# Optimization experiments

Measured on AMD Instinct MI355X. Metric: run time of the kernel, lower is better.

## Reference

```python
import jax, jax.numpy as jnp
import numpy as np

HIDDEN = 32
FEATURES = 16
LABELS = 4
T = 8
N = 40000
E = 640000
D_IN = FEATURES + LABELS + HIDDEN + 1  # GATv2Conv input dim = 53


def setup_inputs() -> dict:
    key = jax.random.key(0)
    ks = jax.random.split(key, 16)
    x = jax.random.normal(ks[0], (T, N, FEATURES), dtype=jnp.float32)
    mask = (jax.random.uniform(ks[1], (N,)) < 0.7).astype(jnp.float32)
    labels = jax.random.normal(ks[2], (N, LABELS), dtype=jnp.float32)
    edge_index = jax.random.randint(ks[3], (2, E), 0, N, dtype=jnp.int32)
    edge_weight = jax.random.uniform(ks[4], (E,), dtype=jnp.float32)
    s = 1.0 / np.sqrt(D_IN)
    # 4 GATv2Conv layers stacked: 0=reset, 1=update, 2=cell, 3=final
    Wl = jax.random.normal(ks[5], (4, HIDDEN, D_IN), dtype=jnp.float32) * s
    bl = jnp.zeros((4, HIDDEN), dtype=jnp.float32)
    Wr = jax.random.normal(ks[6], (4, HIDDEN, D_IN), dtype=jnp.float32) * s
    br = jnp.zeros((4, HIDDEN), dtype=jnp.float32)
    att = jax.random.normal(ks[7], (4, HIDDEN), dtype=jnp.float32) * (1.0 / np.sqrt(HIDDEN))
    bconv = jnp.zeros((4, HIDDEN), dtype=jnp.float32)
    W1 = jax.random.normal(ks[8], (FEATURES, HIDDEN), dtype=jnp.float32) * (1.0 / np.sqrt(HIDDEN))
    b1 = jnp.zeros((FEATURES,), dtype=jnp.float32)
    W2 = jax.random.normal(ks[9], (FEATURES, 2 * HIDDEN), dtype=jnp.float32) * (1.0 / np.sqrt(2 * HIDDEN))
    b2 = jnp.zeros((FEATURES,), dtype=jnp.float32)
    return {"x": x, "mask": mask, "labels": labels, "edge_index": edge_index,
            "edge_weight": edge_weight, "Wl": Wl, "bl": bl, "Wr": Wr, "br": br,
            "att": att, "bconv": bconv, "W1": W1, "b1": b1, "W2": W2, "b2": b2}


def gatv2(xin, src, dst, Wl, bl, Wr, br, att, bconv):
    # GATv2Conv, heads=1, add_self_loops=False (edge_weight unused: lin_edge is None)
    xl = xin @ Wl.T + bl          # [N, H] source transform (message)
    xr = xin @ Wr.T + br          # [N, H] target transform
    z = jax.nn.leaky_relu(xl[src] + xr[dst], 0.2)  # [E, H]
    e = z @ att                   # [E] attention logits
    m = jax.ops.segment_max(e, dst, num_segments=N)
    a = jnp.exp(e - m[dst])
    den = jax.ops.segment_sum(a, dst, num_segments=N)[dst]
    a = a / jnp.where(den > 0, den, 1.0)
    out = jax.ops.segment_sum(a[:, None] * xl[src], dst, num_segments=N)
    return out + bconv


def reference(x, mask, labels, edge_index, edge_weight, Wl, bl, Wr, br, att, bconv, W1, b1, W2, b2):
    src, dst = edge_index[0], edge_index[1]
    mcol = mask[:, None]                       # [N, 1] float, concatenated as a feature
    mbool = mcol > 0.5                         # [N, 1] bool, used for where()
    masked_input = jnp.where(mbool[None], x, 0.0)  # [T, N, F]
    hidden0 = jnp.ones((N, HIDDEN), dtype=x.dtype)
    x2_0 = masked_input[0]

    def step(carry, xt):
        hidden, x2 = carry
        ft = jnp.concatenate([x2, mcol, labels], axis=1)        # [N, F+1+L]
        inp = jnp.concatenate([ft, hidden], axis=1)             # [N, D_IN]
        reset = jax.nn.sigmoid(gatv2(inp, src, dst, Wl[0], bl[0], Wr[0], br[0], att[0], bconv[0]))
        update = jax.nn.sigmoid(gatv2(inp, src, dst, Wl[1], bl[1], Wr[1], br[1], att[1], bconv[1]))
        cin = jnp.concatenate([ft, reset * hidden], axis=1)
        cell = jnp.tanh(gatv2(cin, src, dst, Wl[2], bl[2], Wr[2], br[2], att[2], bconv[2]))
        hidden = update * hidden + (1.0 - update) * cell        # (dropout inactive: eval mode)
        y1 = hidden @ W1.T + b1
        x1 = jnp.where(mbool, xt, y1)
        ft2 = jnp.concatenate([x1, mcol, hidden, labels], axis=1)  # [N, D_IN]
        s = jax.nn.relu(gatv2(ft2, src, dst, Wl[3], bl[3], Wr[3], br[3], att[3], bconv[3]))
        y2 = jnp.concatenate([s, hidden], axis=1) @ W2.T + b2
        x2_new = jnp.where(mbool, xt, y2)
        return (hidden, x2_new), x2_new

    _, out = jax.lax.scan(step, (hidden0, x2_0), masked_input)
    return out  # [T, N, F]
```

## Files before the change

kernel.cpp:

```cpp
#include <hip/hip_runtime.h>
#include <math.h>

#define NN   40000
#define EE   640000
#define HID  32
#define FEAT 16
#define LAB  4
#define TT   8
#define DIN  53
#define WD   (HID * DIN)


__global__ __launch_bounds__(256) void zero_i32(int* __restrict__ p, int n) {
    int i = blockIdx.x * 256 + threadIdx.x;
    if (i < n) p[i] = 0;
}

__global__ __launch_bounds__(256) void hist_kernel(const int* __restrict__ dst,
                                                   int* __restrict__ deg) {
    int e = blockIdx.x * 256 + threadIdx.x;
    if (e < EE) atomicAdd(&deg[dst[e]], 1);
}

__global__ __launch_bounds__(1024) void scan_kernel(const int* __restrict__ deg,
                                                    int* __restrict__ row_ptr) {
    __shared__ int wsum[16];
    __shared__ int chunk_total;
    int tid = threadIdx.x;
    int lane = tid & 63, wv = tid >> 6;
    int carry = 0;
    if (tid == 0) row_ptr[0] = 0;
    for (int base = 0; base < NN; base += 1024) {
        int i = base + tid;
        int v = (i < NN) ? deg[i] : 0;
        #pragma unroll
        for (int o = 1; o < 64; o <<= 1) {
            int t = __shfl_up(v, o);
            if (lane >= o) v += t;
        }
        if (lane == 63) wsum[wv] = v;
        __syncthreads();
        if (tid < 16) {
            int s = wsum[tid];
            #pragma unroll
            for (int o = 1; o < 16; o <<= 1) {
                int t = __shfl_up(s, o);
                if (tid >= o) s += t;
            }
            wsum[tid] = s;
            if (tid == 15) chunk_total = s;
        }
        __syncthreads();
        int woff = (wv == 0) ? 0 : wsum[wv - 1];
        if (i < NN) row_ptr[i + 1] = carry + woff + v;
        carry += chunk_total;
        __syncthreads();
    }
}

__global__ __launch_bounds__(256) void scatter_kernel(const int* __restrict__ src,
                                                      const int* __restrict__ dst,
                                                      const int* __restrict__ row_ptr,
                                                      int* __restrict__ cursor,
                                                      int* __restrict__ csr_src) {
    int e = blockIdx.x * 256 + threadIdx.x;
    if (e < EE) {
        int d = dst[e];
        int pos = atomicAdd(&cursor[d], 1);
        csr_src[row_ptr[d] + pos] = src[e];
    }
}


__global__ __launch_bounds__(256) void init_kernel(const float* __restrict__ x0,
                                                   const float* __restrict__ mask,
                                                   float* __restrict__ hidden,
                                                   float* __restrict__ x2) {
    int i = blockIdx.x * 256 + threadIdx.x;
    if (i < NN * HID) hidden[i] = 1.0f;
    if (i < NN * FEAT) {
        int node = i >> 4;
        x2[i] = (mask[node] > 0.5f) ? x0[i] : 0.0f;
    }
}


__global__ __launch_bounds__(256) void dense01_kernel(const float* __restrict__ feat,
                                                      const float* __restrict__ mask,
                                                      const float* __restrict__ labels,
                                                      const float* __restrict__ hsrc,
                                                      const float* __restrict__ Wl,
                                                      const float* __restrict__ bl,
                                                      const float* __restrict__ Wr,
                                                      const float* __restrict__ br,
                                                      float* __restrict__ xl01,
                                                      float* __restrict__ xr01) {
    __shared__ float W_s[4 * WD];
    __shared__ float inp_s[8][DIN];
    for (int idx = threadIdx.x; idx < WD; idx += 256) {
        W_s[idx]          = Wl[idx];
        W_s[WD + idx]     = Wl[WD + idx];
        W_s[2 * WD + idx] = Wr[idx];
        W_s[3 * WD + idx] = Wr[WD + idx];
    }
    int ni = threadIdx.x >> 5, k = threadIdx.x & 31;
    int node = blockIdx.x * 8 + ni;
    for (int i = k; i < DIN; i += 32) {
        float v;
        if (i < 16)       v = feat[node * 16 + i];
        else if (i == 16) v = mask[node];
        else if (i < 21)  v = labels[node * 4 + (i - 17)];
        else              v = hsrc[node * 32 + (i - 21)];
        inp_s[ni][i] = v;
    }
    __syncthreads();
    float l0 = bl[k], l1 = bl[HID + k], r0 = br[k], r1 = br[HID + k];
    const float* w0 = &W_s[k * DIN];
    const float* w1 = &W_s[WD + k * DIN];
    const float* w2 = &W_s[2 * WD + k * DIN];
    const float* w3 = &W_s[3 * WD + k * DIN];
#pragma unroll
    for (int i = 0; i < DIN; ++i) {
        float xv = inp_s[ni][i];
        l0 += xv * w0[i];
        l1 += xv * w1[i];
        r0 += xv * w2[i];
        r1 += xv * w3[i];
    }
    xl01[node * 64 + k]      = l0;
    xl01[node * 64 + 32 + k] = l1;
    xr01[node * 64 + k]      = r0;
    xr01[node * 64 + 32 + k] = r1;
}


__global__ __launch_bounds__(256) void dense_kernel(const float* __restrict__ feat,
                                                    const float* __restrict__ mask,
                                                    const float* __restrict__ labels,
                                                    const float* __restrict__ hsrc,
                                                    const float* __restrict__ hmul,
                                                    const float* __restrict__ Wl,
                                                    const float* __restrict__ bl,
                                                    const float* __restrict__ Wr,
                                                    const float* __restrict__ br,
                                                    float* __restrict__ xl,
                                                    float* __restrict__ xr) {
    __shared__ float Wl_s[WD];
    __shared__ float Wr_s[WD];
    __shared__ float inp_s[8][DIN];
    for (int idx = threadIdx.x; idx < WD; idx += 256) {
        Wl_s[idx] = Wl[idx];
        Wr_s[idx] = Wr[idx];
    }
    int ni = threadIdx.x >> 5, k = threadIdx.x & 31;
    int node = blockIdx.x * 8 + ni;
    for (int i = k; i < DIN; i += 32) {
        float v;
        if (i < 16)       v = feat[node * 16 + i];
        else if (i == 16) v = mask[node];
        else if (i < 21)  v = labels[node * 4 + (i - 17)];
        else              v = hsrc[node * 32 + (i - 21)] * hmul[node * 32 + (i - 21)];
        inp_s[ni][i] = v;
    }
    __syncthreads();
    float al = bl[k], ar = br[k];
    const float* wlr = &Wl_s[k * DIN];
    const float* wrr = &Wr_s[k * DIN];
#pragma unroll
    for (int i = 0; i < DIN; ++i) {
        float xv = inp_s[ni][i];
        al += xv * wlr[i];
        ar += xv * wrr[i];
    }
    xl[node * 32 + k] = al;
    xr[node * 32 + k] = ar;
}


__device__ __forceinline__ float edge_score(const float4& v0, const float4& v1,
                                            const float4& xr0, const float4& xr1,
                                            const float4& at0, const float4& at1) {
    float part, z;
    z = v0.x + xr0.x; z = (z > 0.f) ? z : 0.2f * z; part  = z * at0.x;
    z = v0.y + xr0.y; z = (z > 0.f) ? z : 0.2f * z; part += z * at0.y;
    z = v0.z + xr0.z; z = (z > 0.f) ? z : 0.2f * z; part += z * at0.z;
    z = v0.w + xr0.w; z = (z > 0.f) ? z : 0.2f * z; part += z * at0.w;
    z = v1.x + xr1.x; z = (z > 0.f) ? z : 0.2f * z; part += z * at1.x;
    z = v1.y + xr1.y; z = (z > 0.f) ? z : 0.2f * z; part += z * at1.y;
    z = v1.z + xr1.z; z = (z > 0.f) ? z : 0.2f * z; part += z * at1.z;
    z = v1.w + xr1.w; z = (z > 0.f) ? z : 0.2f * z; part += z * at1.w;
    part += __shfl_xor(part, 1);
    part += __shfl_xor(part, 2);
    return part;
}

__device__ __forceinline__ void online_update(float e, float& m, float& den, float* acc,
                                              const float4& v0, const float4& v1) {
    if (e > m) {
        float sc = __expf(m - e);
        den *= sc;
#pragma unroll
        for (int i = 0; i < 8; ++i) acc[i] *= sc;
        m = e;
    }
    float a = __expf(e - m);
    den += a;
    acc[0] += a * v0.x; acc[1] += a * v0.y; acc[2] += a * v0.z; acc[3] += a * v0.w;
    acc[4] += a * v1.x; acc[5] += a * v1.y; acc[6] += a * v1.z; acc[7] += a * v1.w;
}

__device__ __forceinline__ void merge_groups(float m, float den, const float* acc,
                                             bool nonempty, float* o) {
    if (nonempty) {
        float mt = m;
        mt = fmaxf(mt, __shfl_xor(mt, 4));
        mt = fmaxf(mt, __shfl_xor(mt, 8));
        mt = fmaxf(mt, __shfl_xor(mt, 16));
        mt = fmaxf(mt, __shfl_xor(mt, 32));
        float sc = __expf(m - mt);
        float d = den * sc;
        d += __shfl_xor(d, 4);
        d += __shfl_xor(d, 8);
        d += __shfl_xor(d, 16);
        d += __shfl_xor(d, 32);
#pragma unroll
        for (int i = 0; i < 8; ++i) {
            float t = acc[i] * sc;
            t += __shfl_xor(t, 4);
            t += __shfl_xor(t, 8);
            t += __shfl_xor(t, 16);
            t += __shfl_xor(t, 32);
            o[i] = t / d;
        }
    } else {
#pragma unroll
        for (int i = 0; i < 8; ++i) o[i] = 0.0f;
    }
}


__global__ __launch_bounds__(256) void conv01_kernel(const int* __restrict__ row_ptr,
                                                     const int* __restrict__ csr_src,
                                                     const float* __restrict__ xl01,
                                                     const float* __restrict__ xr01,
                                                     const float* __restrict__ att,
                                                     const float* __restrict__ bconv,
                                                     float* __restrict__ g0,
                                                     float* __restrict__ g1) {
    int wid  = threadIdx.x >> 6;
    int lane = threadIdx.x & 63;
    int g = lane >> 2, j = lane & 3;
    int n = blockIdx.x * 4 + wid;
    int c0 = j * 8;
    int beg = row_ptr[n], end = row_ptr[n + 1];

    float4 a00 = *(const float4*)(att + c0);
    float4 a01 = *(const float4*)(att + c0 + 4);
    float4 a10 = *(const float4*)(att + 32 + c0);
    float4 a11 = *(const float4*)(att + 32 + c0 + 4);
    const float* xrn = xr01 + n * 64;
    float4 xr00 = *(const float4*)(xrn + c0);
    float4 xr01v = *(const float4*)(xrn + c0 + 4);
    float4 xr10 = *(const float4*)(xrn + 32 + c0);
    float4 xr11 = *(const float4*)(xrn + 32 + c0 + 4);

    float m0 = -INFINITY, den0 = 0.0f, acc0[8] = {0, 0, 0, 0, 0, 0, 0, 0};
    float m1 = -INFINITY, den1 = 0.0f, acc1[8] = {0, 0, 0, 0, 0, 0, 0, 0};

    for (int p = beg + g; p < end; p += 16) {
        int s = csr_src[p];
        const float4* rp = (const float4*)(xl01 + s * 64 + c0);
        const float4* rq = (const float4*)(xl01 + s * 64 + 32 + c0);
        float4 v00 = rp[0], v01 = rp[1];
        float4 v10 = rq[0], v11 = rq[1];
        float e0 = edge_score(v00, v01, xr00, xr01v, a00, a01);
        float e1 = edge_score(v10, v11, xr10, xr11, a10, a11);
        online_update(e0, m0, den0, acc0, v00, v01);
        online_update(e1, m1, den1, acc1, v10, v11);
    }

    float o0[8], o1[8];
    bool ne = beg < end;
    merge_groups(m0, den0, acc0, ne, o0);
    merge_groups(m1, den1, acc1, ne, o1);

    if (g == 0) {
        float4 b00 = *(const float4*)(bconv + c0);
        float4 b01 = *(const float4*)(bconv + c0 + 4);
        float4 b10 = *(const float4*)(bconv + 32 + c0);
        float4 b11 = *(const float4*)(bconv + 32 + c0 + 4);
        float r0[8] = {o0[0] + b00.x, o0[1] + b00.y, o0[2] + b00.z, o0[3] + b00.w,
                       o0[4] + b01.x, o0[5] + b01.y, o0[6] + b01.z, o0[7] + b01.w};
        float r1[8] = {o1[0] + b10.x, o1[1] + b10.y, o1[2] + b10.z, o1[3] + b10.w,
                       o1[4] + b11.x, o1[5] + b11.y, o1[6] + b11.z, o1[7] + b11.w};
#pragma unroll
        for (int i = 0; i < 8; ++i) {
            r0[i] = 1.0f / (1.0f + __expf(-r0[i]));
            r1[i] = 1.0f / (1.0f + __expf(-r1[i]));
        }
        float4* p0 = (float4*)(g0 + n * 32 + c0);
        p0[0] = make_float4(r0[0], r0[1], r0[2], r0[3]);
        p0[1] = make_float4(r0[4], r0[5], r0[6], r0[7]);
        float4* p1 = (float4*)(g1 + n * 32 + c0);
        p1[0] = make_float4(r1[0], r1[1], r1[2], r1[3]);
        p1[1] = make_float4(r1[4], r1[5], r1[6], r1[7]);
    }
}


__global__ __launch_bounds__(256) void conv2_kernel(const int* __restrict__ row_ptr,
                                                    const int* __restrict__ csr_src,
                                                    const float* __restrict__ xl,
                                                    const float* __restrict__ xr,
                                                    const float* __restrict__ att,
                                                    const float* __restrict__ bconv,
                                                    float* __restrict__ out) {
    int wid  = threadIdx.x >> 6;
    int lane = threadIdx.x & 63;
    int g = lane >> 2, j = lane & 3;
    int n = blockIdx.x * 4 + wid;
    int c0 = j * 8;
    int beg = row_ptr[n], end = row_ptr[n + 1];

    float4 at0 = *(const float4*)(att + c0);
    float4 at1 = *(const float4*)(att + c0 + 4);
    float4 xr0 = *(const float4*)(xr + n * 32 + c0);
    float4 xr1 = *(const float4*)(xr + n * 32 + c0 + 4);

    float m = -INFINITY, den = 0.0f, acc[8] = {0, 0, 0, 0, 0, 0, 0, 0};
    for (int p = beg + g; p < end; p += 16) {
        int s = csr_src[p];
        const float4* rp = (const float4*)(xl + s * 32 + c0);
        float4 v0 = rp[0], v1 = rp[1];
        float e = edge_score(v0, v1, xr0, xr1, at0, at1);
        online_update(e, m, den, acc, v0, v1);
    }
    float o[8];
    merge_groups(m, den, acc, beg < end, o);

    if (g == 0) {
        float4 bc0 = *(const float4*)(bconv + c0);
        float4 bc1 = *(const float4*)(bconv + c0 + 4);
        float r[8] = {o[0] + bc0.x, o[1] + bc0.y, o[2] + bc0.z, o[3] + bc0.w,
                      o[4] + bc1.x, o[5] + bc1.y, o[6] + bc1.z, o[7] + bc1.w};
#pragma unroll
        for (int i = 0; i < 8; ++i) r[i] = tanhf(r[i]);
        float4* op = (float4*)(out + n * 32 + c0);
        op[0] = make_float4(r[0], r[1], r[2], r[3]);
        op[1] = make_float4(r[4], r[5], r[6], r[7]);
    }
}


__global__ __launch_bounds__(256) void conv3_out_kernel(const int* __restrict__ row_ptr,
                                                        const int* __restrict__ csr_src,
                                                        const float* __restrict__ xl,
                                                        const float* __restrict__ xr,
                                                        const float* __restrict__ att,
                                                        const float* __restrict__ bconv,
                                                        const float* __restrict__ hidden,
                                                        const float* __restrict__ W2,
                                                        const float* __restrict__ b2,
                                                        const float* __restrict__ x_t,
                                                        const float* __restrict__ mask,
                                                        float* __restrict__ x2,
                                                        float* __restrict__ out_t) {
    __shared__ float W2s[64 * 16];
    for (int idx = threadIdx.x; idx < 64 * 16; idx += 256) {
        int f = idx & 15, c = idx >> 4;
        W2s[c * 16 + f] = W2[f * 64 + c];
    }
    __syncthreads();

    int wid  = threadIdx.x >> 6;
    int lane = threadIdx.x & 63;
    int g = lane >> 2, j = lane & 3;
    int n = blockIdx.x * 4 + wid;
    int c0 = j * 8;
    int beg = row_ptr[n], end = row_ptr[n + 1];

    float4 at0 = *(const float4*)(att + c0);
    float4 at1 = *(const float4*)(att + c0 + 4);
    float4 xr0 = *(const float4*)(xr + n * 32 + c0);
    float4 xr1 = *(const float4*)(xr + n * 32 + c0 + 4);

    float m = -INFINITY, den = 0.0f, acc[8] = {0, 0, 0, 0, 0, 0, 0, 0};
    for (int p = beg + g; p < end; p += 16) {
        int s = csr_src[p];
        const float4* rp = (const float4*)(xl + s * 32 + c0);
        float4 v0 = rp[0], v1 = rp[1];
        float e = edge_score(v0, v1, xr0, xr1, at0, at1);
        online_update(e, m, den, acc, v0, v1);
    }
    float o[8];
    merge_groups(m, den, acc, beg < end, o);

    float4 bc0 = *(const float4*)(bconv + c0);
    float4 bc1 = *(const float4*)(bconv + c0 + 4);
    float r[8] = {fmaxf(o[0] + bc0.x, 0.f), fmaxf(o[1] + bc0.y, 0.f),
                  fmaxf(o[2] + bc0.z, 0.f), fmaxf(o[3] + bc0.w, 0.f),
                  fmaxf(o[4] + bc1.x, 0.f), fmaxf(o[5] + bc1.y, 0.f),
                  fmaxf(o[6] + bc1.z, 0.f), fmaxf(o[7] + bc1.w, 0.f)};
    float4 h0 = *(const float4*)(hidden + n * 32 + c0);
    float4 h1 = *(const float4*)(hidden + n * 32 + c0 + 4);
    float hv[8] = {h0.x, h0.y, h0.z, h0.w, h1.x, h1.y, h1.z, h1.w};

    int f = lane & 15;
    int base = lane & ~3;
    float y = b2[f];
#pragma unroll
    for (int j2 = 0; j2 < 4; ++j2) {
#pragma unroll
        for (int i = 0; i < 8; ++i) {
            float sv = __shfl(r[i], base + j2);
            float hh = __shfl(hv[i], base + j2);
            int c = j2 * 8 + i;
            y += sv * W2s[c * 16 + f] + hh * W2s[(32 + c) * 16 + f];
        }
    }
    if (lane < 16) {
        float mv = mask[n];
        float xv = x_t[n * 16 + f];
        float rr = (mv > 0.5f) ? xv : y;
        x2[n * 16 + f] = rr;
        out_t[n * 16 + f] = rr;
    }
}


__global__ __launch_bounds__(256) void update_dense3_kernel(
        const float* __restrict__ g_update, const float* __restrict__ g_cell,
        float* __restrict__ hidden,
        const float* __restrict__ x_t, const float* __restrict__ mask,
        const float* __restrict__ labels,
        const float* __restrict__ W1, const float* __restrict__ b1,
        const float* __restrict__ Wl3, const float* __restrict__ bl3,
        const float* __restrict__ Wr3, const float* __restrict__ br3,
        float* __restrict__ xl, float* __restrict__ xr) {
    __shared__ float Wl_s[WD];
    __shared__ float Wr_s[WD];
    __shared__ float W1_s[FEAT * HID];
    __shared__ float inp_s[8][DIN];
    __shared__ float hs[8][HID + 1];
    for (int idx = threadIdx.x; idx < WD; idx += 256) {
        Wl_s[idx] = Wl3[idx];
        Wr_s[idx] = Wr3[idx];
    }
    for (int idx = threadIdx.x; idx < FEAT * HID; idx += 256) W1_s[idx] = W1[idx];
    int ni = threadIdx.x >> 5, k = threadIdx.x & 31;
    int node = blockIdx.x * 8 + ni;
    float u = g_update[node * 32 + k];
    float c = g_cell[node * 32 + k];
    float h = hidden[node * 32 + k];
    float hn = u * h + (1.0f - u) * c;
    hidden[node * 32 + k] = hn;
    hs[ni][k] = hn;
    inp_s[ni][17 + k] = hn;
    if (k == 0) inp_s[ni][16] = mask[node];
    if (k < 4)  inp_s[ni][49 + k] = labels[node * 4 + k];
    __syncthreads();
    if (k < 16) {
        float a = b1[k];
        const float* w = &W1_s[k * 32];
#pragma unroll
        for (int i = 0; i < 32; ++i) a += hs[ni][i] * w[i];
        float mv = mask[node];
        inp_s[ni][k] = (mv > 0.5f) ? x_t[node * 16 + k] : a;
    }
    __syncthreads();
    float al = bl3[k], ar = br3[k];
    const float* wl = &Wl_s[k * DIN];
    const float* wr = &Wr_s[k * DIN];
#pragma unroll
    for (int i = 0; i < DIN; ++i) {
        float xv = inp_s[ni][i];
        al += xv * wl[i];
        ar += xv * wr[i];
    }
    xl[node * 32 + k] = al;
    xr[node * 32 + k] = ar;
}


extern "C" void kernel_launch(void* const* d_in, const int* in_sizes, int n_in,
                              void* d_out, int out_size, void* d_ws, size_t ws_size,
                              hipStream_t stream) {
    const float* x      = (const float*)d_in[0];
    const float* mask   = (const float*)d_in[1];
    const float* labels = (const float*)d_in[2];
    const int*   src    = (const int*)d_in[3];
    const int*   dst    = src + EE;
    const float* Wl    = (const float*)d_in[5];
    const float* bl    = (const float*)d_in[6];
    const float* Wr    = (const float*)d_in[7];
    const float* br    = (const float*)d_in[8];
    const float* att   = (const float*)d_in[9];
    const float* bconv = (const float*)d_in[10];
    const float* W1    = (const float*)d_in[11];
    const float* b1    = (const float*)d_in[12];
    const float* W2    = (const float*)d_in[13];
    const float* b2    = (const float*)d_in[14];
    float* out = (float*)d_out;

    char* ws = (char*)d_ws;
    size_t off = 0;
    auto alloc = [&](size_t bytes) -> void* {
        void* p = ws + off;
        off = (off + bytes + 255) & ~(size_t)255;
        return p;
    };
    int*   row_ptr = (int*)alloc((NN + 1) * sizeof(int));
    int*   deg     = (int*)alloc(NN * sizeof(int));
    int*   csr_src = (int*)alloc(EE * sizeof(int));
    float* hidden  = (float*)alloc(NN * HID * sizeof(float));
    float* x2      = (float*)alloc(NN * FEAT * sizeof(float));
    float* xl01    = (float*)alloc(NN * 64 * sizeof(float));
    float* xr01    = (float*)alloc(NN * 64 * sizeof(float));
    float* xl      = (float*)alloc(NN * HID * sizeof(float));
    float* xr      = (float*)alloc(NN * HID * sizeof(float));
    float* g0      = (float*)alloc(NN * HID * sizeof(float));
    float* g1      = (float*)alloc(NN * HID * sizeof(float));
    float* g2      = (float*)alloc(NN * HID * sizeof(float));

    zero_i32<<<(NN + 255) / 256, 256, 0, stream>>>(deg, NN);
    hist_kernel<<<EE / 256, 256, 0, stream>>>(dst, deg);
    scan_kernel<<<1, 1024, 0, stream>>>(deg, row_ptr);
    zero_i32<<<(NN + 255) / 256, 256, 0, stream>>>(deg, NN);
    scatter_kernel<<<EE / 256, 256, 0, stream>>>(src, dst, row_ptr, deg, csr_src);
    init_kernel<<<NN * HID / 256, 256, 0, stream>>>(x, mask, hidden, x2);

    for (int t = 0; t < TT; ++t) {
        const float* xt = x + (size_t)t * NN * FEAT;
        float* out_t = out + (size_t)t * NN * FEAT;
        dense01_kernel<<<NN / 8, 256, 0, stream>>>(x2, mask, labels, hidden,
            Wl, bl, Wr, br, xl01, xr01);
        conv01_kernel<<<NN / 4, 256, 0, stream>>>(row_ptr, csr_src, xl01, xr01,
            att, bconv, g0, g1);
        dense_kernel<<<NN / 8, 256, 0, stream>>>(x2, mask, labels, hidden, g0,
            Wl + 2 * WD, bl + 2 * HID, Wr + 2 * WD, br + 2 * HID, xl, xr);
        conv2_kernel<<<NN / 4, 256, 0, stream>>>(row_ptr, csr_src, xl, xr,
            att + 2 * HID, bconv + 2 * HID, g2);
        update_dense3_kernel<<<NN / 8, 256, 0, stream>>>(g1, g2, hidden, xt, mask, labels,
            W1, b1, Wl + 3 * WD, bl + 3 * HID, Wr + 3 * WD, br + 3 * HID, xl, xr);
        conv3_out_kernel<<<NN / 4, 256, 0, stream>>>(row_ptr, csr_src, xl, xr,
            att + 3 * HID, bconv + 3 * HID, hidden, W2, b2, xt, mask, x2, out_t);
    }
}
```

Baseline: 2.052 ms.

## Store gathered source features in bf16 and sort CSR neighbors by source

The xl source-feature tables gathered per edge are now written as bf16 and unpacked to fp32 in the attention kernels. This halves the bytes fetched in the random per-edge gathers. A one-time per-node insertion sort orders each CSR row's source indices, which should improve locality of those gathers. The cost is reduced precision in messages and attention logits, plus an extra setup kernel.

After: 2.176 ms. +6.0%, slower.

```diff
diff --git a/kernel.cpp b/kernel.cpp
--- a/kernel.cpp
+++ b/kernel.cpp
@@ -9,6 +9,21 @@
 #define TT   8
 #define DIN  53
 #define WD   (HID * DIN)
+
+
+__device__ __forceinline__ unsigned short f2bf(float f) {
+    unsigned int u = __float_as_uint(f);
+    unsigned int r = u + 0x7fffu + ((u >> 16) & 1u);
+    return (unsigned short)(r >> 16);
+}
+__device__ __forceinline__ float bflo(unsigned int u) { return __uint_as_float(u << 16); }
+__device__ __forceinline__ float bfhi(unsigned int u) { return __uint_as_float(u & 0xffff0000u); }
+__device__ __forceinline__ void unpack8(uint4 u, float* v) {
+    v[0] = bflo(u.x); v[1] = bfhi(u.x);
+    v[2] = bflo(u.y); v[3] = bfhi(u.y);
+    v[4] = bflo(u.z); v[5] = bfhi(u.z);
+    v[6] = bflo(u.w); v[7] = bfhi(u.w);
+}
 
 
 __global__ __launch_bounds__(256) void zero_i32(int* __restrict__ p, int n) {
@@ -71,6 +86,23 @@
     }
 }
 
+__global__ __launch_bounds__(256) void sort_kernel(const int* __restrict__ row_ptr,
+                                                   int* __restrict__ csr_src) {
+    int n = blockIdx.x * 256 + threadIdx.x;
+    if (n < NN) {
+        int beg = row_ptr[n], end = row_ptr[n + 1];
+        for (int i = beg + 1; i < end; ++i) {
+            int key = csr_src[i];
+            int j = i - 1;
+            while (j >= beg && csr_src[j] > key) {
+                csr_src[j + 1] = csr_src[j];
+                --j;
+            }
+            csr_src[j + 1] = key;
+        }
+    }
+}
+
 
 __global__ __launch_bounds__(256) void init_kernel(const float* __restrict__ x0,
                                                    const float* __restrict__ mask,
@@ -93,7 +125,7 @@
                                                       const float* __restrict__ bl,
                                                       const float* __restrict__ Wr,
                                                       const float* __restrict__ br,
-                                                      float* __restrict__ xl01,
+                                                      unsigned short* __restrict__ xl01h,
                                                       float* __restrict__ xr01) {
     __shared__ float W_s[4 * WD];
     __shared__ float inp_s[8][DIN];
@@ -127,8 +159,8 @@
         r0 += xv * w2[i];
         r1 += xv * w3[i];
     }
-    xl01[node * 64 + k]      = l0;
-    xl01[node * 64 + 32 + k] = l1;
+    xl01h[node * 64 + k]      = f2bf(l0);
+    xl01h[node * 64 + 32 + k] = f2bf(l1);
     xr01[node * 64 + k]      = r0;
     xr01[node * 64 + 32 + k] = r1;
 }
@@ -143,7 +175,7 @@
                                                     const float* __restrict__ bl,
                                                     const float* __restrict__ Wr,
                                                     const float* __restrict__ br,
-                                                    float* __restrict__ xl,
+                                                    unsigned short* __restrict__ xlh,
                                                     float* __restrict__ xr) {
     __shared__ float Wl_s[WD];
     __shared__ float Wr_s[WD];
@@ -172,30 +204,26 @@
         al += xv * wlr[i];
         ar += xv * wrr[i];
     }
-    xl[node * 32 + k] = al;
+    xlh[node * 32 + k] = f2bf(al);
     xr[node * 32 + k] = ar;
 }
 
 
-__device__ __forceinline__ float edge_score(const float4& v0, const float4& v1,
-                                            const float4& xr0, const float4& xr1,
-                                            const float4& at0, const float4& at1) {
-    float part, z;
-    z = v0.x + xr0.x; z = (z > 0.f) ? z : 0.2f * z; part  = z * at0.x;
-    z = v0.y + xr0.y; z = (z > 0.f) ? z : 0.2f * z; part += z * at0.y;
-    z = v0.z + xr0.z; z = (z > 0.f) ? z : 0.2f * z; part += z * at0.z;
-    z = v0.w + xr0.w; z = (z > 0.f) ? z : 0.2f * z; part += z * at0.w;
-    z = v1.x + xr1.x; z = (z > 0.f) ? z : 0.2f * z; part += z * at1.x;
-    z = v1.y + xr1.y; z = (z > 0.f) ? z : 0.2f * z; part += z * at1.y;
-    z = v1.z + xr1.z; z = (z > 0.f) ? z : 0.2f * z; part += z * at1.z;
-    z = v1.w + xr1.w; z = (z > 0.f) ? z : 0.2f * z; part += z * at1.w;
+__device__ __forceinline__ float edge_score8(const float* v, const float* xr, const float* at) {
+    float part = 0.0f;
+#pragma unroll
+    for (int i = 0; i < 8; ++i) {
+        float z = v[i] + xr[i];
+        z = (z > 0.0f) ? z : 0.2f * z;
+        part += z * at[i];
+    }
     part += __shfl_xor(part, 1);
     part += __shfl_xor(part, 2);
     return part;
 }
 
-__device__ __forceinline__ void online_update(float e, float& m, float& den, float* acc,
-                                              const float4& v0, const float4& v1) {
+__device__ __forceinline__ void online_update8(float e, float& m, float& den, float* acc,
+                                               const float* v) {
     if (e > m) {
         float sc = __expf(m - e);
         den *= sc;
@@ -205,13 +233,13 @@
     }
     float a = __expf(e - m);
     den += a;
-    acc[0] += a * v0.x; acc[1] += a * v0.y; acc[2] += a * v0.z; acc[3] += a * v0.w;
-    acc[4] += a * v1.x; acc[5] += a * v1.y; acc[6] += a * v1.z; acc[7] += a * v1.w;
-}
-
-__device__ __forceinline__ void merge_groups(float m, float den, const float* acc,
-                                             bool nonempty, float* o) {
-    if (nonempty) {
+#pragma unroll
+    for (int i = 0; i < 8; ++i) acc[i] += a * v[i];
+}
+
+__device__ __forceinline__ void merge_full(float m, float den, const float* acc,
+                                           bool ne, float* o) {
+    if (ne) {
         float mt = m;
         mt = fmaxf(mt, __shfl_xor(mt, 4));
         mt = fmaxf(mt, __shfl_xor(mt, 8));
@@ -241,7 +269,7 @@
 
 __global__ __launch_bounds__(256) void conv01_kernel(const int* __restrict__ row_ptr,
                                                      const int* __restrict__ csr_src,
-                                                     const float* __restrict__ xl01,
+                                                     const unsigned short* __restrict__ xl01h,
                                                      const float* __restrict__ xr01,
                                                      const float* __restrict__ att,
                                                      const float* __restrict__ bconv,
@@ -254,63 +282,71 @@
     int c0 = j * 8;
     int beg = row_ptr[n], end = row_ptr[n + 1];
 
-    float4 a00 = *(const float4*)(att + c0);
-    float4 a01 = *(const float4*)(att + c0 + 4);
-    float4 a10 = *(const float4*)(att + 32 + c0);
-    float4 a11 = *(const float4*)(att + 32 + c0 + 4);
-    const float* xrn = xr01 + n * 64;
-    float4 xr00 = *(const float4*)(xrn + c0);
-    float4 xr01v = *(const float4*)(xrn + c0 + 4);
-    float4 xr10 = *(const float4*)(xrn + 32 + c0);
-    float4 xr11 = *(const float4*)(xrn + 32 + c0 + 4);
+    float at0v[8], at1v[8], xr0v[8], xr1v[8];
+    {
+        float4 a0 = *(const float4*)(att + c0);
+        float4 a1 = *(const float4*)(att + c0 + 4);
+        at0v[0] = a0.x; at0v[1] = a0.y; at0v[2] = a0.z; at0v[3] = a0.w;
+        at0v[4] = a1.x; at0v[5] = a1.y; at0v[6] = a1.z; at0v[7] = a1.w;
+        float4 b0 = *(const float4*)(att + 32 + c0);
+        float4 b1 = *(const float4*)(att + 32 + c0 + 4);
+        at1v[0] = b0.x; at1v[1] = b0.y; at1v[2] = b0.z; at1v[3] = b0.w;
+        at1v[4] = b1.x; at1v[5] = b1.y; at1v[6] = b1.z; at1v[7] = b1.w;
+        const float* xrn = xr01 + n * 64;
+        float4 r0 = *(const float4*)(xrn + c0);
+        float4 r1 = *(const float4*)(xrn + c0 + 4);
+        xr0v[0] = r0.x; xr0v[1] = r0.y; xr0v[2] = r0.z; xr0v[3] = r0.w;
+        xr0v[4] = r1.x; xr0v[5] = r1.y; xr0v[6] = r1.z; xr0v[7] = r1.w;
+        float4 r2 = *(const float4*)(xrn + 32 + c0);
+        float4 r3 = *(const float4*)(xrn + 32 + c0 + 4);
+        xr1v[0] = r2.x; xr1v[1] = r2.y; xr1v[2] = r2.z; xr1v[3] = r2.w;
+        xr1v[4] = r3.x; xr1v[5] = r3.y; xr1v[6] = r3.z; xr1v[7] = r3.w;
+    }
 
     float m0 = -INFINITY, den0 = 0.0f, acc0[8] = {0, 0, 0, 0, 0, 0, 0, 0};
     float m1 = -INFINITY, den1 = 0.0f, acc1[8] = {0, 0, 0, 0, 0, 0, 0, 0};
 
     for (int p = beg + g; p < end; p += 16) {
         int s = csr_src[p];
-        const float4* rp = (const float4*)(xl01 + s * 64 + c0);
-        const float4* rq = (const float4*)(xl01 + s * 64 + 32 + c0);
-        float4 v00 = rp[0], v01 = rp[1];
-        float4 v10 = rq[0], v11 = rq[1];
-        float e0 = edge_score(v00, v01, xr00, xr01v, a00, a01);
-        float e1 = edge_score(v10, v11, xr10, xr11, a10, a11);
-        online_update(e0, m0, den0, acc0, v00, v01);
-        online_update(e1, m1, den1, acc1, v10, v11);
+        const unsigned short* row = xl01h + (size_t)s * 64;
+        uint4 u0 = *(const uint4*)(row + c0);
+        uint4 u1 = *(const uint4*)(row + 32 + c0);
+        float v0[8], v1[8];
+        unpack8(u0, v0);
+        unpack8(u1, v1);
+        float e0 = edge_score8(v0, xr0v, at0v);
+        float e1 = edge_score8(v1, xr1v, at1v);
+        online_update8(e0, m0, den0, acc0, v0);
+        online_update8(e1, m1, den1, acc1, v1);
     }
 
     float o0[8], o1[8];
     bool ne = beg < end;
-    merge_groups(m0, den0, acc0, ne, o0);
-    merge_groups(m1, den1, acc1, ne, o1);
+    merge_full(m0, den0, acc0, ne, o0);
+    merge_full(m1, den1, acc1, ne, o1);
 
     if (g == 0) {
-        float4 b00 = *(const float4*)(bconv + c0);
-        float4 b01 = *(const float4*)(bconv + c0 + 4);
-        float4 b10 = *(const float4*)(bconv + 32 + c0);
-        float4 b11 = *(const float4*)(bconv + 32 + c0 + 4);
-        float r0[8] = {o0[0] + b00.x, o0[1] + b00.y, o0[2] + b00.z, o0[3] + b00.w,
-                       o0[4] + b01.x, o0[5] + b01.y, o0[6] + b01.z, o0[7] + b01.w};
-        float r1[8] = {o1[0] + b10.x, o1[1] + b10.y, o1[2] + b10.z, o1[3] + b10.w,
-                       o1[4] + b11.x, o1[5] + b11.y, o1[6] + b11.z, o1[7] + b11.w};
+        const float* bc0 = bconv + c0;
+        const float* bc1 = bconv + 32 + c0;
+        float r0[8], r1[8];
 #pragma unroll
         for (int i = 0; i < 8; ++i) {
-            r0[i] = 1.0f / (1.0f + __expf(-r0[i]));
-            r1[i] = 1.0f / (1.0f + __expf(-r1[i]));
+            r0[i] = 1.0f / (1.0f + __expf(-(o0[i] + bc0[i])));
+            r1[i] = 1.0f / (1.0f + __expf(-(o1[i] + bc1[i])));
         }
-        float4* p0 = (float4*)(g0 + n * 32 + c0);
-        p0[0] = make_float4(r0[0], r0[1], r0[2], r0[3]);
-        p0[1] = make_float4(r0[4], r0[5], r0[6], r0[7]);
-        float4* p1 = (float4*)(g1 + n * 32 + c0);
-        p1[0] = make_float4(r1[0], r1[1], r1[2], r1[3]);
-        p1[1] = make_float4(r1[4], r1[5], r1[6], r1[7]);
+        float* p0 = g0 + n * 32 + c0;
+        ((float4*)p0)[0] = make_float4(r0[0], r0[1], r0[2], r0[3]);
+        ((float4*)p0)[1] = make_float4(r0[4], r0[5], r0[6], r0[7]);
+        float* p1 = g1 + n * 32 + c0;
+        ((float4*)p1)[0] = make_float4(r1[0], r1[1], r1[2], r1[3]);
+        ((float4*)p1)[1] = make_float4(r1[4], r1[5], r1[6], r1[7]);
     }
 }
 
 
 __global__ __launch_bounds__(256) void conv2_kernel(const int* __restrict__ row_ptr,
                                                     const int* __restrict__ csr_src,
-                                                    const float* __restrict__ xl,
+                                                    const unsigned short* __restrict__ xlh,
                                                     const float* __restrict__ xr,
                                                     const float* __restrict__ att,
                                                     const float* __restrict__ bconv,
@@ -322,39 +358,45 @@
     int c0 = j * 8;
     int beg = row_ptr[n], end = row_ptr[n + 1];
 
-    float4 at0 = *(const float4*)(att + c0);
-    float4 at1 = *(const float4*)(att + c0 + 4);
-    float4 xr0 = *(const float4*)(xr + n * 32 + c0);
-    float4 xr1 = *(const float4*)(xr + n * 32 + c0 + 4);
+    float at[8], xrv[8];
+    {
+        float4 a0 = *(const float4*)(att + c0);
+        float4 a1 = *(const float4*)(att + c0 + 4);
+        at[0] = a0.x; at[1] = a0.y; at[2] = a0.z; at[3] = a0.w;
+        at[4] = a1.x; at[5] = a1.y; at[6] = a1.z; at[7] = a1.w;
+        float4 r0 = *(const float4*)(xr + n * 32 + c0);
+        float4 r1 = *(const float4*)(xr + n * 32 + c0 + 4);
+        xrv[0] = r0.x; xrv[1] = r0.y; xrv[2] = r0.z; xrv[3] = r0.w;
+        xrv[4] = r1.x; xrv[5] = r1.y; xrv[6] = r1.z; xrv[7] = r1.w;
+    }
 
     float m = -INFINITY, den = 0.0f, acc[8] = {0, 0, 0, 0, 0, 0, 0, 0};
     for (int p = beg + g; p < end; p += 16) {
         int s = csr_src[p];
-        const float4* rp = (const float4*)(xl + s * 32 + c0);
-        float4 v0 = rp[0], v1 = rp[1];
-        float e = edge_score(v0, v1, xr0, xr1, at0, at1);
-        online_update(e, m, den, acc, v0, v1);
+        uint4 u = *(const uint4*)(xlh + (size_t)s * 32 + c0);
+        float v[8];
+        unpack8(u, v);
+        float e = edge_score8(v, xrv, at);
+        online_update8(e, m, den, acc, v);
     }
     float o[8];
-    merge_groups(m, den, acc, beg < end, o);
+    merge_full(m, den, acc, beg < end, o);
 
     if (g == 0) {
-        float4 bc0 = *(const float4*)(bconv + c0);
-        float4 bc1 = *(const float4*)(bconv + c0 + 4);
-        float r[8] = {o[0] + bc0.x, o[1] + bc0.y, o[2] + bc0.z, o[3] + bc0.w,
-                      o[4] + bc1.x, o[5] + bc1.y, o[6] + bc1.z, o[7] + bc1.w};
-#pragma unroll
-        for (int i = 0; i < 8; ++i) r[i] = tanhf(r[i]);
-        float4* op = (float4*)(out + n * 32 + c0);
-        op[0] = make_float4(r[0], r[1], r[2], r[3]);
-        op[1] = make_float4(r[4], r[5], r[6], r[7]);
+        const float* bc = bconv + c0;
+        float r[8];
+#pragma unroll
+        for (int i = 0; i < 8; ++i) r[i] = tanhf(o[i] + bc[i]);
+        float* op = out + n * 32 + c0;
+        ((float4*)op)[0] = make_float4(r[0], r[1], r[2], r[3]);
+        ((float4*)op)[1] = make_float4(r[4], r[5], r[6], r[7]);
     }
 }
 
 
 __global__ __launch_bounds__(256) void conv3_out_kernel(const int* __restrict__ row_ptr,
                                                         const int* __restrict__ csr_src,
-                                                        const float* __restrict__ xl,
+                                                        const unsigned short* __restrict__ xlh,
                                                         const float* __restrict__ xr,
                                                         const float* __restrict__ att,
                                                         const float* __restrict__ bconv,
@@ -379,31 +421,40 @@
     int c0 = j * 8;
     int beg = row_ptr[n], end = row_ptr[n + 1];
 
-    float4 at0 = *(const float4*)(att + c0);
-    float4 at1 = *(const float4*)(att + c0 + 4);
-    float4 xr0 = *(const float4*)(xr + n * 32 + c0);
-    float4 xr1 = *(const float4*)(xr + n * 32 + c0 + 4);
+    float at[8], xrv[8];
+    {
+        float4 a0 = *(const float4*)(att + c0);
+        float4 a1 = *(const float4*)(att + c0 + 4);
+        at[0] = a0.x; at[1] = a0.y; at[2] = a0.z; at[3] = a0.w;
+        at[4] = a1.x; at[5] = a1.y; at[6] = a1.z; at[7] = a1.w;
+        float4 r0 = *(const float4*)(xr + n * 32 + c0);
+        float4 r1 = *(const float4*)(xr + n * 32 + c0 + 4);
+        xrv[0] = r0.x; xrv[1] = r0.y; xrv[2] = r0.z; xrv[3] = r0.w;
+        xrv[4] = r1.x; xrv[5] = r1.y; xrv[6] = r1.z; xrv[7] = r1.w;
+    }
 
     float m = -INFINITY, den = 0.0f, acc[8] = {0, 0, 0, 0, 0, 0, 0, 0};
     for (int p = beg + g; p < end; p += 16) {
         int s = csr_src[p];
-        const float4* rp = (const float4*)(xl + s * 32 + c0);
-        float4 v0 = rp[0], v1 = rp[1];
-        float e = edge_score(v0, v1, xr0, xr1, at0, at1);
-        online_update(e, m, den, acc, v0, v1);
+        uint4 u = *(const uint4*)(xlh + (size_t)s * 32 + c0);
+        float v[8];
+        unpack8(u, v);
+        float e = edge_score8(v, xrv, at);
+        online_update8(e, m, den, acc, v);
     }
     float o[8];
-    merge_groups(m, den, acc, beg < end, o);
-
-    float4 bc0 = *(const float4*)(bconv + c0);
-    float4 bc1 = *(const float4*)(bconv + c0 + 4);
-    float r[8] = {fmaxf(o[0] + bc0.x, 0.f), fmaxf(o[1] + bc0.y, 0.f),
-                  fmaxf(o[2] + bc0.z, 0.f), fmaxf(o[3] + bc0.w, 0.f),
-                  fmaxf(o[4] + bc1.x, 0.f), fmaxf(o[5] + bc1.y, 0.f),
-                  fmaxf(o[6] + bc1.z, 0.f), fmaxf(o[7] + bc1.w, 0.f)};
-    float4 h0 = *(const float4*)(hidden + n * 32 + c0);
-    float4 h1 = *(const float4*)(hidden + n * 32 + c0 + 4);
-    float hv[8] = {h0.x, h0.y, h0.z, h0.w, h1.x, h1.y, h1.z, h1.w};
+    merge_full(m, den, acc, beg < end, o);
+
+    float r[8], hv[8];
+    {
+        const float* bc = bconv + c0;
+#pragma unroll
+        for (int i = 0; i < 8; ++i) r[i] = fmaxf(o[i] + bc[i], 0.0f);
+        float4 h0 = *(const float4*)(hidden + n * 32 + c0);
+        float4 h1 = *(const float4*)(hidden + n * 32 + c0 + 4);
+        hv[0] = h0.x; hv[1] = h0.y; hv[2] = h0.z; hv[3] = h0.w;
+        hv[4] = h1.x; hv[5] = h1.y; hv[6] = h1.z; hv[7] = h1.w;
+    }
 
     int f = lane & 15;
     int base = lane & ~3;
@@ -436,7 +487,7 @@
         const float* __restrict__ W1, const float* __restrict__ b1,
         const float* __restrict__ Wl3, const float* __restrict__ bl3,
         const float* __restrict__ Wr3, const float* __restrict__ br3,
-        float* __restrict__ xl, float* __restrict__ xr) {
+        unsigned short* __restrict__ xlh, float* __restrict__ xr) {
     __shared__ float Wl_s[WD];
     __shared__ float Wr_s[WD];
     __shared__ float W1_s[FEAT * HID];
@@ -477,7 +528,7 @@
         al += xv * wl[i];
         ar += xv * wr[i];
     }
-    xl[node * 32 + k] = al;
+    xlh[node * 32 + k] = f2bf(al);
     xr[node * 32 + k] = ar;
 }
 
@@ -514,9 +565,9 @@
     int*   csr_src = (int*)alloc(EE * sizeof(int));
     float* hidden  = (float*)alloc(NN * HID * sizeof(float));
     float* x2      = (float*)alloc(NN * FEAT * sizeof(float));
-    float* xl01    = (float*)alloc(NN * 64 * sizeof(float));
+    unsigned short* xl01h = (unsigned short*)alloc(NN * 64 * sizeof(unsigned short));
     float* xr01    = (float*)alloc(NN * 64 * sizeof(float));
-    float* xl      = (float*)alloc(NN * HID * sizeof(float));
+    unsigned short* xlh = (unsigned short*)alloc(NN * 32 * sizeof(unsigned short));
     float* xr      = (float*)alloc(NN * HID * sizeof(float));
     float* g0      = (float*)alloc(NN * HID * sizeof(float));
     float* g1      = (float*)alloc(NN * HID * sizeof(float));
@@ -527,22 +578,23 @@
     scan_kernel<<<1, 1024, 0, stream>>>(deg, row_ptr);
     zero_i32<<<(NN + 255) / 256, 256, 0, stream>>>(deg, NN);
     scatter_kernel<<<EE / 256, 256, 0, stream>>>(src, dst, row_ptr, deg, csr_src);
+    sort_kernel<<<(NN + 255) / 256, 256, 0, stream>>>(row_ptr, csr_src);
     init_kernel<<<NN * HID / 256, 256, 0, stream>>>(x, mask, hidden, x2);
 
     for (int t = 0; t < TT; ++t) {
         const float* xt = x + (size_t)t * NN * FEAT;
         float* out_t = out + (size_t)t * NN * FEAT;
         dense01_kernel<<<NN / 8, 256, 0, stream>>>(x2, mask, labels, hidden,
-            Wl, bl, Wr, br, xl01, xr01);
-        conv01_kernel<<<NN / 4, 256, 0, stream>>>(row_ptr, csr_src, xl01, xr01,
+            Wl, bl, Wr, br, xl01h, xr01);
+        conv01_kernel<<<NN / 4, 256, 0, stream>>>(row_ptr, csr_src, xl01h, xr01,
             att, bconv, g0, g1);
         dense_kernel<<<NN / 8, 256, 0, stream>>>(x2, mask, labels, hidden, g0,
-            Wl + 2 * WD, bl + 2 * HID, Wr + 2 * WD, br + 2 * HID, xl, xr);
-        conv2_kernel<<<NN / 4, 256, 0, stream>>>(row_ptr, csr_src, xl, xr,
+            Wl + 2 * WD, bl + 2 * HID, Wr + 2 * WD, br + 2 * HID, xlh, xr);
+        conv2_kernel<<<NN / 4, 256, 0, stream>>>(row_ptr, csr_src, xlh, xr,
             att + 2 * HID, bconv + 2 * HID, g2);
         update_dense3_kernel<<<NN / 8, 256, 0, stream>>>(g1, g2, hidden, xt, mask, labels,
-            W1, b1, Wl + 3 * WD, bl + 3 * HID, Wr + 3 * WD, br + 3 * HID, xl, xr);
-        conv3_out_kernel<<<NN / 4, 256, 0, stream>>>(row_ptr, csr_src, xl, xr,
+            W1, b1, Wl + 3 * WD, bl + 3 * HID, Wr + 3 * WD, br + 3 * HID, xlh, xr);
+        conv3_out_kernel<<<NN / 4, 256, 0, stream>>>(row_ptr, csr_src, xlh, xr,
             att + 3 * HID, bconv + 3 * HID, hidden, W2, b2, xt, mask, x2, out_t);
     }
 }
```
